# Kernel optimization log

Measured on AMD Instinct MI355X. Metric: run time of the kernel, lower is better.

Reference implementation:

```python
import jax, jax.numpy as jnp
import numpy as np

B, N, F_IN, HID, HEADS = 4, 10000, 128, 64, 4
E = 160000
NEG_SLOPE = 0.2


def _glorot(key, shape):
    fan_in, fan_out = shape[0], shape[-1]
    lim = jnp.sqrt(6.0 / (fan_in + fan_out)).astype(jnp.float32)
    return jax.random.uniform(key, shape, jnp.float32, -lim, lim)


def setup_inputs() -> dict:
    key = jax.random.key(0)
    ks = jax.random.split(key, 10)
    x = jax.random.normal(ks[0], (B, N, F_IN), jnp.float32)
    edge_index = jax.random.randint(ks[1], (2, E), 0, N, dtype=jnp.int32)
    return {
        "x": x,
        "edge_index": edge_index,
        "W1": _glorot(ks[2], (F_IN, HEADS * HID)),
        "a_src1": _glorot(ks[3], (HEADS, HID)),
        "a_dst1": _glorot(ks[4], (HEADS, HID)),
        "b1": jnp.zeros((HID,), jnp.float32),
        "W2": _glorot(ks[5], (HID, HEADS * HID)),
        "a_src2": _glorot(ks[6], (HEADS, HID)),
        "a_dst2": _glorot(ks[7], (HEADS, HID)),
        "b2": jnp.zeros((HID,), jnp.float32),
    }


def gat_conv(x, src, dst, W, a_src, a_dst, b):
    # x: [N, F]; src/dst: [E'] (self-loops already appended)
    h = (x @ W).reshape(N, HEADS, HID)              # [N, H, C]
    al_src = jnp.einsum("nhc,hc->nh", h, a_src)      # [N, H]
    al_dst = jnp.einsum("nhc,hc->nh", h, a_dst)
    e = jax.nn.leaky_relu(al_src[src] + al_dst[dst], NEG_SLOPE)  # [E', H]
    # segment softmax over incoming edges per destination node
    m = jax.ops.segment_max(e, dst, num_segments=N)  # [N, H]
    e = jnp.exp(e - m[dst])
    s = jax.ops.segment_sum(e, dst, num_segments=N)
    alpha = e / (s[dst] + 1e-16)                     # [E', H]
    out = jax.ops.segment_sum(alpha[:, :, None] * h[src], dst, num_segments=N)  # [N, H, C]
    return out.mean(axis=1) + b                      # concat=False -> head mean


def reference(x, edge_index, W1, a_src1, a_dst1, b1, W2, a_src2, a_dst2, b2):
    loops = jnp.arange(N, dtype=edge_index.dtype)
    src = jnp.concatenate([edge_index[0], loops])
    dst = jnp.concatenate([edge_index[1], loops])

    conv1 = jax.vmap(lambda xi: gat_conv(xi, src, dst, W1, a_src1, a_dst1, b1))
    conv2 = jax.vmap(lambda xi: gat_conv(xi, src, dst, W2, a_src2, a_dst2, b2))

    h = conv1(x)                 # [B, N, HID]
    h = jax.nn.elu(h)
    h = conv2(h)
    return h
```

## Files before the change

kernel.cpp:

```cpp
#include <hip/hip_runtime.h>
#include <hip/hip_fp16.h>
#include <math.h>

#define N_NODES 10000
#define N_PAD 10240
#define B_BATCH 4
#define F_IN_C 128
#define HID_C 64
#define E_EDGES 160000
#define E_TOT (E_EDGES + N_NODES)
#define E_OCT 240000
#define NEG_SLOPE 0.2f
#define LOG2E 1.44269504f
#define SN (N_NODES + 8)
#define SH (N_NODES + 8)

typedef _Float16 half8 __attribute__((ext_vector_type(8)));
typedef float f32x4 __attribute__((ext_vector_type(4)));


__global__ void k_zero(int* __restrict__ deg) {
    deg[blockIdx.x * 256 + threadIdx.x] = 0;
}


__device__ void wext_body(const float* __restrict__ W, const float* __restrict__ asrc,
                          const float* __restrict__ adst, __half* __restrict__ Wt,
                          int tid, int K) {
    int nc = tid / K, k = tid % K;
    float v;
    if (nc < 256) {
        v = W[k * 256 + nc];
    } else if (nc < 260) {
        int hd = nc - 256; v = 0.f;
        for (int c = 0; c < 64; c++) v += W[k * 256 + hd * 64 + c] * asrc[hd * 64 + c];
        v *= LOG2E;
    } else if (nc < 264) {
        int hd = nc - 260; v = 0.f;
        for (int c = 0; c < 64; c++) v += W[k * 256 + hd * 64 + c] * adst[hd * 64 + c];
        v *= LOG2E;
    } else {
        v = 0.f;
    }
    Wt[(size_t)nc * K + k] = __float2half(v);
}


__global__ void k_setup(const float* __restrict__ W1, const float* __restrict__ as1,
                        const float* __restrict__ ad1, const float* __restrict__ W2,
                        const float* __restrict__ as2, const float* __restrict__ ad2,
                        __half* __restrict__ Wt1, __half* __restrict__ Wt2,
                        int* __restrict__ csr_b, __half* __restrict__ h2,
                        float* __restrict__ alsrc, int* __restrict__ deg,
                        const int* __restrict__ ei) {
    int blk = blockIdx.x, t = threadIdx.x;
    if (blk < 136) {
        wext_body(W1, as1, ad1, Wt1, blk * 256 + t, F_IN_C);
    } else if (blk < 204) {
        wext_body(W2, as2, ad2, Wt2, (blk - 136) * 256 + t, HID_C);
    } else if (blk < 1142) {
        int i = (blk - 204) * 256 + t;
        if (i < E_OCT) csr_b[i] = N_NODES << 9;
    } else if (blk == 1142) {
        for (int i = t; i < 4 * 256; i += 256) {
            int b = i >> 8, c = i & 255;
            h2[((size_t)b * SH + N_NODES) * 256 + c] = __float2half(0.f);
        }
        if (t < 16) {
            int b = t >> 2, q = t & 3;
            alsrc[((size_t)b * SN + N_NODES) * 4 + q] = -1e30f;
        }
    } else {
        int e = (blk - 1143) * 256 + t;
        if (e < E_EDGES) atomicAdd(&deg[ei[E_EDGES + e]], 1);
    }
}


template <int K, typename XT>
__device__ void gemm_body(const XT* __restrict__ x, const __half* __restrict__ Wt,
                          __half* __restrict__ h2, float* __restrict__ alsrc,
                          float* __restrict__ aldst, int b, int tile) {
    int t = threadIdx.x;
    int w = t >> 6, lane = t & 63;
    int node0 = tile * 16;
    int col = lane & 15, kblk = lane >> 4;

    const XT* xr = x + ((size_t)b * N_NODES + node0 + col) * K + kblk * 8;

    f32x4 acc0 = {0.f, 0.f, 0.f, 0.f};
    f32x4 acc1 = {0.f, 0.f, 0.f, 0.f};
    f32x4 acc2 = {0.f, 0.f, 0.f, 0.f};
    f32x4 acc3 = {0.f, 0.f, 0.f, 0.f};
    f32x4 accal = {0.f, 0.f, 0.f, 0.f};

#pragma unroll
    for (int k0 = 0; k0 < K; k0 += 32) {
        half8 a;
        if constexpr (sizeof(XT) == 4) {
            float4 xa = *(const float4*)(xr + k0);
            float4 xc = *(const float4*)(xr + k0 + 4);
            a[0] = (_Float16)xa.x; a[1] = (_Float16)xa.y; a[2] = (_Float16)xa.z; a[3] = (_Float16)xa.w;
            a[4] = (_Float16)xc.x; a[5] = (_Float16)xc.y; a[6] = (_Float16)xc.z; a[7] = (_Float16)xc.w;
        } else {
            a = *(const half8*)(xr + k0);
        }
        const __half* wtk = Wt + kblk * 8 + k0;
        half8 b0 = *(const half8*)(wtk + (size_t)((w * 4 + 0) * 16 + col) * K);
        half8 b1 = *(const half8*)(wtk + (size_t)((w * 4 + 1) * 16 + col) * K);
        half8 b2 = *(const half8*)(wtk + (size_t)((w * 4 + 2) * 16 + col) * K);
        half8 b3 = *(const half8*)(wtk + (size_t)((w * 4 + 3) * 16 + col) * K);
        acc0 = __builtin_amdgcn_mfma_f32_16x16x32_f16(a, b0, acc0, 0, 0, 0);
        acc1 = __builtin_amdgcn_mfma_f32_16x16x32_f16(a, b1, acc1, 0, 0, 0);
        acc2 = __builtin_amdgcn_mfma_f32_16x16x32_f16(a, b2, acc2, 0, 0, 0);
        acc3 = __builtin_amdgcn_mfma_f32_16x16x32_f16(a, b3, acc3, 0, 0, 0);
        if (w == 0) {
            half8 bal = *(const half8*)(wtk + (size_t)(256 + col) * K);
            accal = __builtin_amdgcn_mfma_f32_16x16x32_f16(a, bal, accal, 0, 0, 0);
        }
    }

    {
        __half* dst = h2 + ((size_t)b * SH + node0 + kblk * 4) * 256 + w * 64 + col;
#pragma unroll
        for (int r = 0; r < 4; r++) dst[(size_t)r * 256 + 0 * 16] = __float2half(acc0[r]);
#pragma unroll
        for (int r = 0; r < 4; r++) dst[(size_t)r * 256 + 1 * 16] = __float2half(acc1[r]);
#pragma unroll
        for (int r = 0; r < 4; r++) dst[(size_t)r * 256 + 2 * 16] = __float2half(acc2[r]);
#pragma unroll
        for (int r = 0; r < 4; r++) dst[(size_t)r * 256 + 3 * 16] = __float2half(acc3[r]);
    }
    if (w == 0 && col < 8) {
        int node = node0 + kblk * 4;
        if (col < 4) {
            float* d = alsrc + ((size_t)b * SN + node) * 4 + col;
#pragma unroll
            for (int r = 0; r < 4; r++) d[r * 4] = accal[r];
        } else {
            float* d = aldst + ((size_t)b * SN + node) * 4 + (col - 4);
#pragma unroll
            for (int r = 0; r < 4; r++) d[r * 4] = accal[r];
        }
    }
}


__device__ void scan_body(const int* __restrict__ deg, int* __restrict__ offs,
                          int* __restrict__ cursor) {
    __shared__ int lds[256];
    int t = threadIdx.x;
    int i0 = t * 40;
    int v[40];
#pragma unroll
    for (int q = 0; q < 10; q++) {
        int4 d4 = *(const int4*)(deg + i0 + q * 4);
        v[q * 4 + 0] = (d4.x + 8) & ~7;
        v[q * 4 + 1] = (d4.y + 8) & ~7;
        v[q * 4 + 2] = (d4.z + 8) & ~7;
        v[q * 4 + 3] = (d4.w + 8) & ~7;
    }
    int tot = 0;
#pragma unroll
    for (int j = 0; j < 40; j++) tot += v[j];
    lds[t] = tot;
    __syncthreads();
    for (int ofs = 1; ofs < 256; ofs <<= 1) {
        int w = (t >= ofs) ? lds[t - ofs] : 0;
        __syncthreads();
        lds[t] += w;
        __syncthreads();
    }
    int run = lds[t] - tot;
#pragma unroll
    for (int j = 0; j < 40; j++) {
        int i = i0 + j;
        if (i < N_NODES) {
            cursor[i] = run;
            offs[i + 1] = run + v[j];
        }
        run += v[j];
    }
    if (t == 0) offs[0] = 0;
}


__launch_bounds__(256)
__global__ void k_gemm1_scan(const float* __restrict__ x, const __half* __restrict__ Wt,
                             __half* __restrict__ h2, float* __restrict__ alsrc,
                             float* __restrict__ aldst, const int* __restrict__ deg,
                             int* __restrict__ offs, int* __restrict__ cursor) {
    int bid = blockIdx.x;
    if (bid == 0) { scan_body(deg, offs, cursor); return; }
    gemm_body<F_IN_C, float>(x, Wt, h2, alsrc, aldst, (bid - 1) / 625, (bid - 1) % 625);
}

__launch_bounds__(256)
__global__ void k_gemm2(const __half* __restrict__ x2, const __half* __restrict__ Wt,
                        __half* __restrict__ h2, float* __restrict__ alsrc,
                        float* __restrict__ aldst) {
    gemm_body<HID_C, __half>(x2, Wt, h2, alsrc, aldst, blockIdx.y, blockIdx.x);
}


__global__ void k_scatter(const int* __restrict__ ei, int* __restrict__ cursor,
                          int* __restrict__ csr_b) {
    int e = blockIdx.x * 256 + threadIdx.x;
    if (e < E_TOT) {
        int s, d;
        if (e < E_EDGES) { s = ei[e]; d = ei[E_EDGES + e]; }
        else { s = d = e - E_EDGES; }
        int pos = atomicAdd(&cursor[d], 1);
        csr_b[pos] = s << 9;
    }
}


#define EDGE_FMA(av, g)                                                                   \
    {                                                                                     \
        float v_ = av + ad_h;                                                             \
        v_ = fmaxf(v_, NEG_SLOPE * v_);                                                   \
        float e_;                                                                         \
        asm("v_exp_f32 %0, %1" : "=v"(e_) : "v"(v_));                                     \
        asm("v_fma_mix_f32 %0, %1, %2, %0 op_sel:[0,0,0] op_sel_hi:[1,0,0]"               \
            : "+v"(acc.x) : "v"(g.x), "v"(e_));                                           \
        asm("v_fma_mix_f32 %0, %1, %2, %0 op_sel:[1,0,0] op_sel_hi:[1,0,0]"               \
            : "+v"(acc.y) : "v"(g.x), "v"(e_));                                           \
        asm("v_fma_mix_f32 %0, %1, %2, %0 op_sel:[0,0,0] op_sel_hi:[1,0,0]"               \
            : "+v"(acc.z) : "v"(g.y), "v"(e_));                                           \
        asm("v_fma_mix_f32 %0, %1, %2, %0 op_sel:[1,0,0] op_sel_hi:[1,0,0]"               \
            : "+v"(acc.w) : "v"(g.y), "v"(e_));                                           \
        sacc += e_;                                                                       \
    }

template <bool LAYER1>
__launch_bounds__(256)
__global__ void k_agg(const __half* __restrict__ h2, const float* __restrict__ alsrc,
                      const float* __restrict__ aldst, const int* __restrict__ offs,
                      const int* __restrict__ csr_b, const float* __restrict__ bias,
                      void* __restrict__ outv) {
    int t = threadIdx.x;
    int bid = blockIdx.x;
    int xcd = bid & 7;
    int b = xcd >> 1;
    int local = (bid >> 3) * 2 + (xcd & 1);
    int wv = t >> 6, lane = t & 63;
    int hd = lane >> 4, cl = lane & 15;
    int dst = local * 4 + wv;

    const char* hcb = (const char*)(h2 + (size_t)b * SH * 256);
    const float* als = alsrc + (size_t)b * SN * 4 + hd;
    float ad_h = aldst[((size_t)b * SN + dst) * 4 + hd];
    int s0 = offs[dst], s1 = offs[dst + 1];
    int laneoff = (hd << 7) | (cl << 3);

    float4 acc = make_float4(0.f, 0.f, 0.f, 0.f);
    float sacc = 0.f;
    int4 cA = *(const int4*)(csr_b + s0);
    int4 cB = *(const int4*)(csr_b + s0 + 4);
    uint2 g0 = *(const uint2*)(hcb + (unsigned)(cA.x + laneoff));
    uint2 g1 = *(const uint2*)(hcb + (unsigned)(cA.y + laneoff));
    uint2 g2 = *(const uint2*)(hcb + (unsigned)(cA.z + laneoff));
    uint2 g3 = *(const uint2*)(hcb + (unsigned)(cA.w + laneoff));
    uint2 g4 = *(const uint2*)(hcb + (unsigned)(cB.x + laneoff));
    uint2 g5 = *(const uint2*)(hcb + (unsigned)(cB.y + laneoff));
    uint2 g6 = *(const uint2*)(hcb + (unsigned)(cB.z + laneoff));
    uint2 g7 = *(const uint2*)(hcb + (unsigned)(cB.w + laneoff));
    float a0 = als[cA.x >> 7], a1 = als[cA.y >> 7], a2 = als[cA.z >> 7], a3 = als[cA.w >> 7];
    float a4 = als[cB.x >> 7], a5 = als[cB.y >> 7], a6 = als[cB.z >> 7], a7 = als[cB.w >> 7];
    int jn = (s0 + 8 < s1) ? s0 + 8 : s0;
    int4 cA2 = *(const int4*)(csr_b + jn);
    int4 cB2 = *(const int4*)(csr_b + jn + 4);

    for (int j = s0 + 8; j < s1; j += 8) {
        uint2 m0 = *(const uint2*)(hcb + (unsigned)(cA2.x + laneoff));
        uint2 m1 = *(const uint2*)(hcb + (unsigned)(cA2.y + laneoff));
        uint2 m2 = *(const uint2*)(hcb + (unsigned)(cA2.z + laneoff));
        uint2 m3 = *(const uint2*)(hcb + (unsigned)(cA2.w + laneoff));
        uint2 m4 = *(const uint2*)(hcb + (unsigned)(cB2.x + laneoff));
        uint2 m5 = *(const uint2*)(hcb + (unsigned)(cB2.y + laneoff));
        uint2 m6 = *(const uint2*)(hcb + (unsigned)(cB2.z + laneoff));
        uint2 m7 = *(const uint2*)(hcb + (unsigned)(cB2.w + laneoff));
        float v0 = als[cA2.x >> 7], v1 = als[cA2.y >> 7], v2 = als[cA2.z >> 7], v3 = als[cA2.w >> 7];
        float v4 = als[cB2.x >> 7], v5 = als[cB2.y >> 7], v6 = als[cB2.z >> 7], v7 = als[cB2.w >> 7];
        int j2 = (j + 8 < s1) ? j + 8 : j;
        int4 cA3 = *(const int4*)(csr_b + j2);
        int4 cB3 = *(const int4*)(csr_b + j2 + 4);
        EDGE_FMA(a0, g0) EDGE_FMA(a1, g1) EDGE_FMA(a2, g2) EDGE_FMA(a3, g3)
        EDGE_FMA(a4, g4) EDGE_FMA(a5, g5) EDGE_FMA(a6, g6) EDGE_FMA(a7, g7)
        g0 = m0; g1 = m1; g2 = m2; g3 = m3; g4 = m4; g5 = m5; g6 = m6; g7 = m7;
        a0 = v0; a1 = v1; a2 = v2; a3 = v3; a4 = v4; a5 = v5; a6 = v6; a7 = v7;
        cA2 = cA3; cB2 = cB3;
    }
    EDGE_FMA(a0, g0) EDGE_FMA(a1, g1) EDGE_FMA(a2, g2) EDGE_FMA(a3, g3)
    EDGE_FMA(a4, g4) EDGE_FMA(a5, g5) EDGE_FMA(a6, g6) EDGE_FMA(a7, g7)

    float inv = 1.f / (sacc + 1e-16f);
    float4 v = make_float4(acc.x * inv, acc.y * inv, acc.z * inv, acc.w * inv);
#pragma unroll
    for (int o = 16; o < 64; o <<= 1) {
        v.x += __shfl_xor(v.x, o);
        v.y += __shfl_xor(v.y, o);
        v.z += __shfl_xor(v.z, o);
        v.w += __shfl_xor(v.w, o);
    }
    if (lane < 16) {
        float4 b4 = *(const float4*)(bias + cl * 4);
        float ox = v.x * 0.25f + b4.x;
        float oy = v.y * 0.25f + b4.y;
        float oz = v.z * 0.25f + b4.z;
        float ow = v.w * 0.25f + b4.w;
        if (LAYER1) {
            ox = ox > 0.f ? ox : expm1f(ox);
            oy = oy > 0.f ? oy : expm1f(oy);
            oz = oz > 0.f ? oz : expm1f(oz);
            ow = ow > 0.f ? ow : expm1f(ow);
            __half2 lo = __floats2half2_rn(ox, oy);
            __half2 hi = __floats2half2_rn(oz, ow);
            uint2 pk = make_uint2(*(unsigned*)&lo, *(unsigned*)&hi);
            *(uint2*)((__half*)outv + ((size_t)b * N_NODES + dst) * 64 + cl * 4) = pk;
        } else {
            *(float4*)((float*)outv + ((size_t)b * N_NODES + dst) * 64 + cl * 4) =
                make_float4(ox, oy, oz, ow);
        }
    }
}


extern "C" void kernel_launch(void* const* d_in, const int* in_sizes, int n_in,
                              void* d_out, int out_size, void* d_ws, size_t ws_size,
                              hipStream_t stream) {
    const float* x = (const float*)d_in[0];
    const int* ei = (const int*)d_in[1];
    const float* W1 = (const float*)d_in[2];
    const float* as1 = (const float*)d_in[3];
    const float* ad1 = (const float*)d_in[4];
    const float* b1 = (const float*)d_in[5];
    const float* W2 = (const float*)d_in[6];
    const float* as2 = (const float*)d_in[7];
    const float* ad2 = (const float*)d_in[8];
    const float* b2 = (const float*)d_in[9];
    float* out = (float*)d_out;

    char* p = (char*)d_ws;
    int* deg = (int*)p;            p += sizeof(int) * N_PAD;
    int* offs = (int*)p;           p += sizeof(int) * (N_NODES + 4);
    int* cursor = (int*)p;         p += sizeof(int) * N_NODES;
    int* csr_b = (int*)p;          p += sizeof(int) * E_OCT;
    __half* Wt1 = (__half*)p;      p += sizeof(__half) * 272 * F_IN_C;
    __half* Wt2 = (__half*)p;      p += sizeof(__half) * 272 * HID_C;
    float* alsrc = (float*)p;      p += sizeof(float) * B_BATCH * SN * 4;
    float* aldst = (float*)p;      p += sizeof(float) * B_BATCH * SN * 4;
    __half* h2 = (__half*)p;       p += sizeof(__half) * (size_t)B_BATCH * SH * 256;
    __half* x2 = (__half*)p;       p += sizeof(__half) * (size_t)B_BATCH * N_NODES * 64;

    k_zero<<<N_PAD / 256, 256, 0, stream>>>(deg);
    k_setup<<<1768, 256, 0, stream>>>(W1, as1, ad1, W2, as2, ad2, Wt1, Wt2,
                                      csr_b, h2, alsrc, deg, ei);
    k_gemm1_scan<<<2501, 256, 0, stream>>>(x, Wt1, h2, alsrc, aldst, deg, offs, cursor);
    k_scatter<<<(E_TOT + 255) / 256, 256, 0, stream>>>(ei, cursor, csr_b);
    k_agg<true><<<B_BATCH * 2500, 256, 0, stream>>>(h2, alsrc, aldst, offs, csr_b, b1, x2);
    k_gemm2<<<dim3(625, B_BATCH), 256, 0, stream>>>(x2, Wt2, h2, alsrc, aldst);
    k_agg<false><<<B_BATCH * 2500, 256, 0, stream>>>(h2, alsrc, aldst, offs, csr_b, b2, out);
}
```

Measured before the change: 179.4 us.

## Pre-gather per-edge source attention scores into contiguous edge-ordered array

Adds a kernel that, for each CSR edge slot and batch, gathers the four per-head source attention logits into a head-major, edge-ordered buffer. The aggregation kernels then read these with contiguous float4 loads instead of eight scattered per-edge gathers from alsrc. This removes random small loads from the latency-bound aggregation loop. In exchange it adds two extra launches and extra global traffic to write and read a 4*4*E_OCT float buffer.

Result: slower. 191.6 us (+6.8%).

```diff
diff --git a/kernel.cpp b/kernel.cpp
--- a/kernel.cpp
+++ b/kernel.cpp
@@ -216,6 +216,21 @@
 }
 
 
+__global__ void k_alse(const int* __restrict__ csr_b, const float* __restrict__ alsrc,
+                       float* __restrict__ alse) {
+    int j = blockIdx.x * 256 + threadIdx.x;
+    if (j >= E_OCT) return;
+    int b = blockIdx.y;
+    int src4 = csr_b[j] >> 7;
+    float4 a4 = *(const float4*)(alsrc + (size_t)b * SN * 4 + src4);
+    size_t base = (size_t)b * 4 * E_OCT + j;
+    alse[base] = a4.x;
+    alse[base + E_OCT] = a4.y;
+    alse[base + (size_t)2 * E_OCT] = a4.z;
+    alse[base + (size_t)3 * E_OCT] = a4.w;
+}
+
+
 #define EDGE_FMA(av, g)                                                                   \
     {                                                                                     \
         float v_ = av + ad_h;                                                             \
@@ -235,7 +250,7 @@
 
 template <bool LAYER1>
 __launch_bounds__(256)
-__global__ void k_agg(const __half* __restrict__ h2, const float* __restrict__ alsrc,
+__global__ void k_agg(const __half* __restrict__ h2, const float* __restrict__ alse,
                       const float* __restrict__ aldst, const int* __restrict__ offs,
                       const int* __restrict__ csr_b, const float* __restrict__ bias,
                       void* __restrict__ outv) {
@@ -249,7 +264,7 @@
     int dst = local * 4 + wv;
 
     const char* hcb = (const char*)(h2 + (size_t)b * SH * 256);
-    const float* als = alsrc + (size_t)b * SN * 4 + hd;
+    const float* aep = alse + (size_t)(b * 4 + hd) * E_OCT;
     float ad_h = aldst[((size_t)b * SN + dst) * 4 + hd];
     int s0 = offs[dst], s1 = offs[dst + 1];
     int laneoff = (hd << 7) | (cl << 3);
@@ -258,6 +273,8 @@
     float sacc = 0.f;
     int4 cA = *(const int4*)(csr_b + s0);
     int4 cB = *(const int4*)(csr_b + s0 + 4);
+    float4 pA = *(const float4*)(aep + s0);
+    float4 pB = *(const float4*)(aep + s0 + 4);
     uint2 g0 = *(const uint2*)(hcb + (unsigned)(cA.x + laneoff));
     uint2 g1 = *(const uint2*)(hcb + (unsigned)(cA.y + laneoff));
     uint2 g2 = *(const uint2*)(hcb + (unsigned)(cA.z + laneoff));
@@ -266,11 +283,11 @@
     uint2 g5 = *(const uint2*)(hcb + (unsigned)(cB.y + laneoff));
     uint2 g6 = *(const uint2*)(hcb + (unsigned)(cB.z + laneoff));
     uint2 g7 = *(const uint2*)(hcb + (unsigned)(cB.w + laneoff));
-    float a0 = als[cA.x >> 7], a1 = als[cA.y >> 7], a2 = als[cA.z >> 7], a3 = als[cA.w >> 7];
-    float a4 = als[cB.x >> 7], a5 = als[cB.y >> 7], a6 = als[cB.z >> 7], a7 = als[cB.w >> 7];
     int jn = (s0 + 8 < s1) ? s0 + 8 : s0;
     int4 cA2 = *(const int4*)(csr_b + jn);
     int4 cB2 = *(const int4*)(csr_b + jn + 4);
+    float4 pA2 = *(const float4*)(aep + jn);
+    float4 pB2 = *(const float4*)(aep + jn + 4);
 
     for (int j = s0 + 8; j < s1; j += 8) {
         uint2 m0 = *(const uint2*)(hcb + (unsigned)(cA2.x + laneoff));
@@ -281,19 +298,19 @@
         uint2 m5 = *(const uint2*)(hcb + (unsigned)(cB2.y + laneoff));
         uint2 m6 = *(const uint2*)(hcb + (unsigned)(cB2.z + laneoff));
         uint2 m7 = *(const uint2*)(hcb + (unsigned)(cB2.w + laneoff));
-        float v0 = als[cA2.x >> 7], v1 = als[cA2.y >> 7], v2 = als[cA2.z >> 7], v3 = als[cA2.w >> 7];
-        float v4 = als[cB2.x >> 7], v5 = als[cB2.y >> 7], v6 = als[cB2.z >> 7], v7 = als[cB2.w >> 7];
         int j2 = (j + 8 < s1) ? j + 8 : j;
         int4 cA3 = *(const int4*)(csr_b + j2);
         int4 cB3 = *(const int4*)(csr_b + j2 + 4);
-        EDGE_FMA(a0, g0) EDGE_FMA(a1, g1) EDGE_FMA(a2, g2) EDGE_FMA(a3, g3)
-        EDGE_FMA(a4, g4) EDGE_FMA(a5, g5) EDGE_FMA(a6, g6) EDGE_FMA(a7, g7)
+        float4 pA3 = *(const float4*)(aep + j2);
+        float4 pB3 = *(const float4*)(aep + j2 + 4);
+        EDGE_FMA(pA.x, g0) EDGE_FMA(pA.y, g1) EDGE_FMA(pA.z, g2) EDGE_FMA(pA.w, g3)
+        EDGE_FMA(pB.x, g4) EDGE_FMA(pB.y, g5) EDGE_FMA(pB.z, g6) EDGE_FMA(pB.w, g7)
         g0 = m0; g1 = m1; g2 = m2; g3 = m3; g4 = m4; g5 = m5; g6 = m6; g7 = m7;
-        a0 = v0; a1 = v1; a2 = v2; a3 = v3; a4 = v4; a5 = v5; a6 = v6; a7 = v7;
-        cA2 = cA3; cB2 = cB3;
-    }
-    EDGE_FMA(a0, g0) EDGE_FMA(a1, g1) EDGE_FMA(a2, g2) EDGE_FMA(a3, g3)
-    EDGE_FMA(a4, g4) EDGE_FMA(a5, g5) EDGE_FMA(a6, g6) EDGE_FMA(a7, g7)
+        pA = pA2; pB = pB2;
+        cA2 = cA3; cB2 = cB3; pA2 = pA3; pB2 = pB3;
+    }
+    EDGE_FMA(pA.x, g0) EDGE_FMA(pA.y, g1) EDGE_FMA(pA.z, g2) EDGE_FMA(pA.w, g3)
+    EDGE_FMA(pB.x, g4) EDGE_FMA(pB.y, g5) EDGE_FMA(pB.z, g6) EDGE_FMA(pB.w, g7)
 
     float inv = 1.f / (sacc + 1e-16f);
     float4 v = make_float4(acc.x * inv, acc.y * inv, acc.z * inv, acc.w * inv);
@@ -353,13 +370,18 @@
     float* aldst = (float*)p;      p += sizeof(float) * B_BATCH * SN * 4;
     __half* h2 = (__half*)p;       p += sizeof(__half) * (size_t)B_BATCH * SH * 256;
     __half* x2 = (__half*)p;       p += sizeof(__half) * (size_t)B_BATCH * N_NODES * 64;
+    float* alse = (float*)p;       p += sizeof(float) * (size_t)B_BATCH * 4 * E_OCT;
+
+    dim3 gAlse((E_OCT + 255) / 256, B_BATCH);
 
     k_zero<<<N_PAD / 256, 256, 0, stream>>>(deg);
     k_setup<<<1768, 256, 0, stream>>>(W1, as1, ad1, W2, as2, ad2, Wt1, Wt2,
                                       csr_b, h2, alsrc, deg, ei);
     k_gemm1_scan<<<2501, 256, 0, stream>>>(x, Wt1, h2, alsrc, aldst, deg, offs, cursor);
     k_scatter<<<(E_TOT + 255) / 256, 256, 0, stream>>>(ei, cursor, csr_b);
-    k_agg<true><<<B_BATCH * 2500, 256, 0, stream>>>(h2, alsrc, aldst, offs, csr_b, b1, x2);
+    k_alse<<<gAlse, 256, 0, stream>>>(csr_b, alsrc, alse);
+    k_agg<true><<<B_BATCH * 2500, 256, 0, stream>>>(h2, alse, aldst, offs, csr_b, b1, x2);
     k_gemm2<<<dim3(625, B_BATCH), 256, 0, stream>>>(x2, Wt2, h2, alsrc, aldst);
-    k_agg<false><<<B_BATCH * 2500, 256, 0, stream>>>(h2, alsrc, aldst, offs, csr_b, b2, out);
-}
+    k_alse<<<gAlse, 256, 0, stream>>>(csr_b, alsrc, alse);
+    k_agg<false><<<B_BATCH * 2500, 256, 0, stream>>>(h2, alse, aldst, offs, csr_b, b2, out);
+}
```
